# Kernel optimization log

Measured on AMD Instinct MI355X. Metric: run time of the kernel, lower is better.

Reference implementation:

```python
import jax, jax.numpy as jnp
import numpy as np

COST_CLASS, COST_BBOX, COST_GIOU = 2.0, 5.0, 2.0
ALPHA, GAMMA, EPS = 0.25, 2.0, 1e-8


def box_cxcywh_to_xyxy(b):
    cx, cy, w, h = b[..., 0], b[..., 1], b[..., 2], b[..., 3]
    return jnp.stack([cx - 0.5 * w, cy - 0.5 * h, cx + 0.5 * w, cy + 0.5 * h], axis=-1)


def generalized_box_iou(boxes1, boxes2):
    # boxes1: [N,4] xyxy, boxes2: [M,4] xyxy -> [N,M]
    area1 = (boxes1[:, 2] - boxes1[:, 0]) * (boxes1[:, 3] - boxes1[:, 1])
    area2 = (boxes2[:, 2] - boxes2[:, 0]) * (boxes2[:, 3] - boxes2[:, 1])
    lt = jnp.maximum(boxes1[:, None, :2], boxes2[None, :, :2])
    rb = jnp.minimum(boxes1[:, None, 2:], boxes2[None, :, 2:])
    wh = jnp.clip(rb - lt, 0.0)
    inter = wh[..., 0] * wh[..., 1]
    union = area1[:, None] + area2[None, :] - inter
    iou = inter / union
    lt_c = jnp.minimum(boxes1[:, None, :2], boxes2[None, :, :2])
    rb_c = jnp.maximum(boxes1[:, None, 2:], boxes2[None, :, 2:])
    wh_c = jnp.clip(rb_c - lt_c, 0.0)
    area_c = wh_c[..., 0] * wh_c[..., 1]
    return iou - (area_c - union) / area_c


def setup_inputs() -> dict:
    key = jax.random.key(0)
    k1, k2, k3, k4 = jax.random.split(key, 4)
    return {
        "pred_logits": jax.random.normal(k1, (16, 1000, 256), dtype=jnp.float32),
        "pred_boxes": jax.random.uniform(k2, (16, 1000, 4), dtype=jnp.float32),
        "tgt_labels": jax.random.randint(k3, (1600,), 0, 256, dtype=jnp.int64),
        "tgt_boxes": jax.random.uniform(k4, (1600, 4), dtype=jnp.float32),
    }


def reference(pred_logits, pred_boxes, tgt_labels, tgt_boxes):
    """Computes the [bs, num_queries, M] Hungarian cost matrix C.

    The sequential CPU scipy linear_sum_assignment on C is the post-processing
    step; the kernel-relevant math is the fused cost-matrix construction below.
    """
    bs, nq, nc = pred_logits.shape
    out_prob = jax.nn.sigmoid(pred_logits.reshape(bs * nq, nc))  # [N, C]
    out_bbox = pred_boxes.reshape(bs * nq, 4)                    # [N, 4]
    tgt_ids = jnp.clip(tgt_labels, 0, nc - 1)

    # sigmoid focal class cost
    neg_cost = (1.0 - ALPHA) * out_prob**GAMMA * -jnp.log(1.0 - out_prob + EPS)
    pos_cost = ALPHA * (1.0 - out_prob)**GAMMA * -jnp.log(out_prob + EPS)
    cost_class = pos_cost[:, tgt_ids] - neg_cost[:, tgt_ids]     # [N, M]

    # L1 cdist on cxcywh boxes
    cost_bbox = jnp.abs(out_bbox[:, None, :] - tgt_boxes[None, :, :]).sum(-1)

    # negative generalized IoU
    cost_giou = -generalized_box_iou(box_cxcywh_to_xyxy(out_bbox),
                                     box_cxcywh_to_xyxy(tgt_boxes))

    C = COST_BBOX * cost_bbox + COST_CLASS * cost_class + COST_GIOU * cost_giou
    return C.reshape(bs, nq, -1)
```

## Files before the change

kernel.cpp:

```cpp
#include <hip/hip_runtime.h>


constexpr float ALPHAc = 0.25f;
constexpr float EPSc   = 1e-8f;

constexpr int NC  = 256;
constexpr int NT  = 256;
constexpr int RPB = 8;

typedef float f32x4 __attribute__((ext_vector_type(4)));
typedef float f32x2 __attribute__((ext_vector_type(2)));

struct TBox { float x0, y0, x1, y1, area; };

__device__ __forceinline__ TBox make_box(float4 b) {
    TBox r;
    r.x0 = fmaf(-0.5f, b.z, b.x);
    r.y0 = fmaf(-0.5f, b.w, b.y);
    r.x1 = fmaf( 0.5f, b.z, b.x);
    r.y1 = fmaf( 0.5f, b.w, b.y);
    r.area = b.z * b.w;
    return r;
}

__device__ __forceinline__ const float* fc_base(const float* fc0, int c) {
    c = c < 0 ? 0 : (c > NC - 1 ? NC - 1 : c);
    return fc0 + c;
}

__device__ __forceinline__ float cost_elem(float px0, float py0, float px1, float py1,
                                           float parea, float pw2, float ph2,
                                           const TBox& b, float fcp) {
    const float u0 = b.x0 - px0, u1 = b.x1 - px1;
    const float v0 = b.y0 - py0, v1 = b.y1 - py1;
    const float du = u1 - u0,    dv = v1 - v0;
    const float l1 = fmaf(0.5f, fabsf(u0 + u1), fabsf(du))
                   + fmaf(0.5f, fabsf(v0 + v1), fabsf(dv));
    const float ix0 = fmaxf(px0, b.x0), ix1 = fminf(px1, b.x1);
    const float iy0 = fmaxf(py0, b.y0), iy1 = fminf(py1, b.y1);
    const float iwr = ix1 - ix0, ihr = iy1 - iy0;
    const float inter = fmaxf(iwr, 0.0f) * fmaxf(ihr, 0.0f);
    const float uni   = (parea + b.area) - inter;
    const float cw = (pw2 + du) - iwr;
    const float ch = (ph2 + dv) - ihr;
    const float carea = cw * ch;
    const float num = fmaf(uni, uni, inter * carea);
    const float mm  = num * __builtin_amdgcn_rcpf(uni * carea);
    return fmaf(-2.0f, mm, fmaf(5.0f, l1, fcp));
}

__global__ __launch_bounds__(NT)
void hungarian_cost_kernel(const float* __restrict__ logits,
                           const float* __restrict__ pboxes,
                           const int*   __restrict__ tlabels,
                           const float* __restrict__ tboxes,
                           float*       __restrict__ out,
                           int N, int M)
{
    const int t  = threadIdx.x;
    const int n0 = blockIdx.x * RPB;
    if (n0 >= N) return;
    const int rows = (N - n0 < RPB) ? (N - n0) : RPB;

    __shared__ float fc[RPB][NC];
    __shared__ float pp[RPB][8];

#pragma unroll
    for (int r = 0; r < RPB; ++r) {
        if (r < rows) {
            const float x = logits[(size_t)(n0 + r) * NC + t];
            const float p = __builtin_amdgcn_rcpf(1.0f + __expf(-x));
            const float q = 1.0f - p;
            const float pos = ALPHAc * q * q * (-__logf(p + EPSc));
            const float neg = (1.0f - ALPHAc) * p * p * (-__logf(q + EPSc));
            fc[r][t] = fmaf(2.0f, pos - neg, 2.0f);
        }
    }
    if (t < rows) {
        const float4 pb = reinterpret_cast<const float4*>(pboxes)[n0 + t];
        pp[t][0] = fmaf(-0.5f, pb.z, pb.x);
        pp[t][1] = fmaf(-0.5f, pb.w, pb.y);
        pp[t][2] = fmaf( 0.5f, pb.z, pb.x);
        pp[t][3] = fmaf( 0.5f, pb.w, pb.y);
        pp[t][4] = pb.z * pb.w;
        pp[t][5] = pb.z + pb.z;
        pp[t][6] = pb.w + pb.w;
        pp[t][7] = 0.0f;
    }
    __syncthreads();

    const float4* tb4 = reinterpret_cast<const float4*>(tboxes);
    const float*  fc0 = &fc[0][0];

    const int nA    = (M >> 2) < NT ? (M >> 2) : NT;
    const int baseB = 4 * nA;
    const int nB    = ((M - baseB) >> 1) < NT ? ((M - baseB) >> 1) : NT;
    const int baseC = baseB + 2 * nB;

    if (rows == RPB) {

        if (t < nA) {
            const int4 c4 = reinterpret_cast<const int4*>(tlabels)[t];
            const TBox b0 = make_box(tb4[4 * t + 0]);
            const TBox b1 = make_box(tb4[4 * t + 1]);
            const TBox b2 = make_box(tb4[4 * t + 2]);
            const TBox b3 = make_box(tb4[4 * t + 3]);
            const float* g0 = fc_base(fc0, c4.x);
            const float* g1 = fc_base(fc0, c4.y);
            const float* g2 = fc_base(fc0, c4.z);
            const float* g3 = fc_base(fc0, c4.w);
            float fA[RPB][4];
#pragma unroll
            for (int r = 0; r < RPB; ++r) {
                fA[r][0] = g0[r * NC];
                fA[r][1] = g1[r * NC];
                fA[r][2] = g2[r * NC];
                fA[r][3] = g3[r * NC];
            }
#pragma unroll
            for (int r = 0; r < RPB; ++r) {
                const float4 p0 = *reinterpret_cast<const float4*>(&pp[r][0]);
                const float4 p1 = *reinterpret_cast<const float4*>(&pp[r][4]);
                f32x4 res;
                res.x = cost_elem(p0.x, p0.y, p0.z, p0.w, p1.x, p1.y, p1.z, b0, fA[r][0]);
                res.y = cost_elem(p0.x, p0.y, p0.z, p0.w, p1.x, p1.y, p1.z, b1, fA[r][1]);
                res.z = cost_elem(p0.x, p0.y, p0.z, p0.w, p1.x, p1.y, p1.z, b2, fA[r][2]);
                res.w = cost_elem(p0.x, p0.y, p0.z, p0.w, p1.x, p1.y, p1.z, b3, fA[r][3]);
                float* orow = out + (size_t)(n0 + r) * M;
                __builtin_nontemporal_store(res, reinterpret_cast<f32x4*>(orow) + t);
            }
        }

        if (t < nB) {
            const int2 c2 = reinterpret_cast<const int2*>(tlabels + baseB)[t];
            const TBox b0 = make_box(tb4[baseB + 2 * t + 0]);
            const TBox b1 = make_box(tb4[baseB + 2 * t + 1]);
            const float* g0 = fc_base(fc0, c2.x);
            const float* g1 = fc_base(fc0, c2.y);
            float fB[RPB][2];
#pragma unroll
            for (int r = 0; r < RPB; ++r) {
                fB[r][0] = g0[r * NC];
                fB[r][1] = g1[r * NC];
            }
#pragma unroll
            for (int r = 0; r < RPB; ++r) {
                const float4 p0 = *reinterpret_cast<const float4*>(&pp[r][0]);
                const float4 p1 = *reinterpret_cast<const float4*>(&pp[r][4]);
                f32x2 res;
                res.x = cost_elem(p0.x, p0.y, p0.z, p0.w, p1.x, p1.y, p1.z, b0, fB[r][0]);
                res.y = cost_elem(p0.x, p0.y, p0.z, p0.w, p1.x, p1.y, p1.z, b1, fB[r][1]);
                float* orow = out + (size_t)(n0 + r) * M + baseB;
                __builtin_nontemporal_store(res, reinterpret_cast<f32x2*>(orow) + t);
            }
        }

        if (baseC + t < M) {
            const int e = baseC + t;
            const TBox b = make_box(tb4[e]);
            const float* g = fc_base(fc0, tlabels[e]);
            float fC[RPB];
#pragma unroll
            for (int r = 0; r < RPB; ++r) fC[r] = g[r * NC];
#pragma unroll
            for (int r = 0; r < RPB; ++r) {
                const float4 p0 = *reinterpret_cast<const float4*>(&pp[r][0]);
                const float4 p1 = *reinterpret_cast<const float4*>(&pp[r][4]);
                const float v = cost_elem(p0.x, p0.y, p0.z, p0.w, p1.x, p1.y, p1.z, b, fC[r]);
                __builtin_nontemporal_store(v, out + (size_t)(n0 + r) * M + e);
            }
        }
        for (int e = baseC + NT + t; e < M; e += NT) {
            const TBox b = make_box(tb4[e]);
            const float* g = fc_base(fc0, tlabels[e]);
#pragma unroll
            for (int r = 0; r < RPB; ++r) {
                const float4 p0 = *reinterpret_cast<const float4*>(&pp[r][0]);
                const float4 p1 = *reinterpret_cast<const float4*>(&pp[r][4]);
                const float v = cost_elem(p0.x, p0.y, p0.z, p0.w, p1.x, p1.y, p1.z, b, g[r * NC]);
                __builtin_nontemporal_store(v, out + (size_t)(n0 + r) * M + e);
            }
        }
    } else {
        for (int r = 0; r < rows; ++r) {
            const float4 p0 = *reinterpret_cast<const float4*>(&pp[r][0]);
            const float4 p1 = *reinterpret_cast<const float4*>(&pp[r][4]);
            for (int e = t; e < M; e += NT) {
                const TBox b = make_box(tb4[e]);
                const float f = *fc_base(fc0 + r * NC, tlabels[e]);
                out[(size_t)(n0 + r) * M + e] =
                    cost_elem(p0.x, p0.y, p0.z, p0.w, p1.x, p1.y, p1.z, b, f);
            }
        }
    }
}

extern "C" void kernel_launch(void* const* d_in, const int* in_sizes, int n_in,
                              void* d_out, int out_size, void* d_ws, size_t ws_size,
                              hipStream_t stream) {
    const float* logits  = (const float*)d_in[0];
    const float* pboxes  = (const float*)d_in[1];
    const int*   tlabels = (const int*)d_in[2];
    const float* tboxes  = (const float*)d_in[3];

    float* out = (float*)d_out;

    const int N = in_sizes[1] / 4;
    const int M = in_sizes[2];

    const int nblocks = (N + RPB - 1) / RPB;
    hipLaunchKernelGGL(hungarian_cost_kernel, dim3(nblocks), dim3(NT), 0, stream,
                       logits, pboxes, tlabels, tboxes, out, N, M);
}
```

Baseline: 33.26 us.

## Make cost kernel persistent with double-buffered tiles and prefetched logits

Turns the one-block-per-8-rows launch into a persistent grid capped at 500 workgroups. Each block loops over row tiles, keeps target boxes and labels in registers across tiles, and prefetches the next tile's logits and pred boxes into registers while computing the current one. The class-cost shared buffer is double-buffered so a single barrier per tile is enough. This is meant to remove repeated per-block setup and hide global-load latency, at the cost of more registers (possibly lower occupancy) and fewer blocks (N=16000 gives 2000 tiles, so about 4 tiles per block).

```diff
diff --git a/kernel.cpp b/kernel.cpp
--- a/kernel.cpp
+++ b/kernel.cpp
@@ -4,9 +4,10 @@
 constexpr float ALPHAc = 0.25f;
 constexpr float EPSc   = 1e-8f;
 
-constexpr int NC  = 256;
-constexpr int NT  = 256;
-constexpr int RPB = 8;
+constexpr int NC    = 256;
+constexpr int NT    = 256;
+constexpr int RPB   = 8;
+constexpr int MAXWG = 500;
 
 typedef float f32x4 __attribute__((ext_vector_type(4)));
 typedef float f32x2 __attribute__((ext_vector_type(2)));
@@ -23,9 +24,8 @@
     return r;
 }
 
-__device__ __forceinline__ const float* fc_base(const float* fc0, int c) {
-    c = c < 0 ? 0 : (c > NC - 1 ? NC - 1 : c);
-    return fc0 + c;
+__device__ __forceinline__ int clamp_cls(int c) {
+    return c < 0 ? 0 : (c > NC - 1 ? NC - 1 : c);
 }
 
 __device__ __forceinline__ float cost_elem(float px0, float py0, float px1, float py1,
@@ -57,141 +57,207 @@
                            float*       __restrict__ out,
                            int N, int M)
 {
-    const int t  = threadIdx.x;
-    const int n0 = blockIdx.x * RPB;
-    if (n0 >= N) return;
-    const int rows = (N - n0 < RPB) ? (N - n0) : RPB;
-
-    __shared__ float fc[RPB][NC];
-    __shared__ float pp[RPB][8];
-
-#pragma unroll
-    for (int r = 0; r < RPB; ++r) {
-        if (r < rows) {
-            const float x = logits[(size_t)(n0 + r) * NC + t];
-            const float p = __builtin_amdgcn_rcpf(1.0f + __expf(-x));
-            const float q = 1.0f - p;
-            const float pos = ALPHAc * q * q * (-__logf(p + EPSc));
-            const float neg = (1.0f - ALPHAc) * p * p * (-__logf(q + EPSc));
-            fc[r][t] = fmaf(2.0f, pos - neg, 2.0f);
-        }
-    }
-    if (t < rows) {
-        const float4 pb = reinterpret_cast<const float4*>(pboxes)[n0 + t];
-        pp[t][0] = fmaf(-0.5f, pb.z, pb.x);
-        pp[t][1] = fmaf(-0.5f, pb.w, pb.y);
-        pp[t][2] = fmaf( 0.5f, pb.z, pb.x);
-        pp[t][3] = fmaf( 0.5f, pb.w, pb.y);
-        pp[t][4] = pb.z * pb.w;
-        pp[t][5] = pb.z + pb.z;
-        pp[t][6] = pb.w + pb.w;
-        pp[t][7] = 0.0f;
-    }
-    __syncthreads();
+    const int t        = threadIdx.x;
+    const int nwg      = gridDim.x;
+    const int numTiles = (N + RPB - 1) / RPB;
+
+    __shared__ float fc[2][RPB][NC];
+    __shared__ float pp[2][RPB][8];
 
     const float4* tb4 = reinterpret_cast<const float4*>(tboxes);
-    const float*  fc0 = &fc[0][0];
+    const float4* pb4 = reinterpret_cast<const float4*>(pboxes);
 
     const int nA    = (M >> 2) < NT ? (M >> 2) : NT;
     const int baseB = 4 * nA;
     const int nB    = ((M - baseB) >> 1) < NT ? ((M - baseB) >> 1) : NT;
     const int baseC = baseB + 2 * nB;
-
-    if (rows == RPB) {
-
-        if (t < nA) {
-            const int4 c4 = reinterpret_cast<const int4*>(tlabels)[t];
-            const TBox b0 = make_box(tb4[4 * t + 0]);
-            const TBox b1 = make_box(tb4[4 * t + 1]);
-            const TBox b2 = make_box(tb4[4 * t + 2]);
-            const TBox b3 = make_box(tb4[4 * t + 3]);
-            const float* g0 = fc_base(fc0, c4.x);
-            const float* g1 = fc_base(fc0, c4.y);
-            const float* g2 = fc_base(fc0, c4.z);
-            const float* g3 = fc_base(fc0, c4.w);
-            float fA[RPB][4];
+    const bool aV = t < nA;
+    const bool bV = t < nB;
+    const bool cV = (baseC + t) < M;
+
+    TBox bA0 = {}, bA1 = {}, bA2 = {}, bA3 = {}, bB0 = {}, bB1 = {}, bC = {};
+    int cA0 = 0, cA1 = 0, cA2 = 0, cA3 = 0, cB0 = 0, cB1 = 0, cC = 0;
+    if (aV) {
+        const int4 c4 = reinterpret_cast<const int4*>(tlabels)[t];
+        bA0 = make_box(tb4[4 * t + 0]);
+        bA1 = make_box(tb4[4 * t + 1]);
+        bA2 = make_box(tb4[4 * t + 2]);
+        bA3 = make_box(tb4[4 * t + 3]);
+        cA0 = clamp_cls(c4.x); cA1 = clamp_cls(c4.y);
+        cA2 = clamp_cls(c4.z); cA3 = clamp_cls(c4.w);
+    }
+    if (bV) {
+        const int2 c2 = reinterpret_cast<const int2*>(tlabels + baseB)[t];
+        bB0 = make_box(tb4[baseB + 2 * t + 0]);
+        bB1 = make_box(tb4[baseB + 2 * t + 1]);
+        cB0 = clamp_cls(c2.x); cB1 = clamp_cls(c2.y);
+    }
+    if (cV) {
+        bC = make_box(tb4[baseC + t]);
+        cC = clamp_cls(tlabels[baseC + t]);
+    }
+
+    int tile = blockIdx.x;
+    if (tile >= numTiles) return;
+
+    float xcur[RPB];
+    float4 pbcur = {0.0f, 0.0f, 0.0f, 0.0f};
+    {
+        const int n0 = tile * RPB;
+#pragma unroll
+        for (int r = 0; r < RPB; ++r) {
+            int n = n0 + r; n = n < N - 1 ? n : N - 1;
+            xcur[r] = logits[(size_t)n * NC + t];
+        }
+        if (t < RPB) {
+            int n = n0 + t; n = n < N - 1 ? n : N - 1;
+            pbcur = pb4[n];
+        }
+    }
+
+    bool bsel = false;
+    for (; tile < numTiles; tile += nwg) {
+        const int n0   = tile * RPB;
+        const int rows = (N - n0 < RPB) ? (N - n0) : RPB;
+        float (*fcb)[NC] = bsel ? fc[1] : fc[0];
+        float (*ppb)[8]  = bsel ? pp[1] : pp[0];
+
+#pragma unroll
+        for (int r = 0; r < RPB; ++r) {
+            if (r < rows) {
+                const float x = xcur[r];
+                const float p = __builtin_amdgcn_rcpf(1.0f + __expf(-x));
+                const float q = 1.0f - p;
+                const float pos = ALPHAc * q * q * (-__logf(p + EPSc));
+                const float neg = (1.0f - ALPHAc) * p * p * (-__logf(q + EPSc));
+                fcb[r][t] = fmaf(2.0f, pos - neg, 2.0f);
+            }
+        }
+        if (t < rows) {
+            const float4 pb = pbcur;
+            ppb[t][0] = fmaf(-0.5f, pb.z, pb.x);
+            ppb[t][1] = fmaf(-0.5f, pb.w, pb.y);
+            ppb[t][2] = fmaf( 0.5f, pb.z, pb.x);
+            ppb[t][3] = fmaf( 0.5f, pb.w, pb.y);
+            ppb[t][4] = pb.z * pb.w;
+            ppb[t][5] = pb.z + pb.z;
+            ppb[t][6] = pb.w + pb.w;
+            ppb[t][7] = 0.0f;
+        }
+        __syncthreads();
+
+        const int ntile = tile + nwg;
+        float xnext[RPB];
+        float4 pbnext = pbcur;
+        if (ntile < numTiles) {
+            const int nn0 = ntile * RPB;
 #pragma unroll
             for (int r = 0; r < RPB; ++r) {
-                fA[r][0] = g0[r * NC];
-                fA[r][1] = g1[r * NC];
-                fA[r][2] = g2[r * NC];
-                fA[r][3] = g3[r * NC];
-            }
-#pragma unroll
-            for (int r = 0; r < RPB; ++r) {
-                const float4 p0 = *reinterpret_cast<const float4*>(&pp[r][0]);
-                const float4 p1 = *reinterpret_cast<const float4*>(&pp[r][4]);
-                f32x4 res;
-                res.x = cost_elem(p0.x, p0.y, p0.z, p0.w, p1.x, p1.y, p1.z, b0, fA[r][0]);
-                res.y = cost_elem(p0.x, p0.y, p0.z, p0.w, p1.x, p1.y, p1.z, b1, fA[r][1]);
-                res.z = cost_elem(p0.x, p0.y, p0.z, p0.w, p1.x, p1.y, p1.z, b2, fA[r][2]);
-                res.w = cost_elem(p0.x, p0.y, p0.z, p0.w, p1.x, p1.y, p1.z, b3, fA[r][3]);
-                float* orow = out + (size_t)(n0 + r) * M;
-                __builtin_nontemporal_store(res, reinterpret_cast<f32x4*>(orow) + t);
-            }
-        }
-
-        if (t < nB) {
-            const int2 c2 = reinterpret_cast<const int2*>(tlabels + baseB)[t];
-            const TBox b0 = make_box(tb4[baseB + 2 * t + 0]);
-            const TBox b1 = make_box(tb4[baseB + 2 * t + 1]);
-            const float* g0 = fc_base(fc0, c2.x);
-            const float* g1 = fc_base(fc0, c2.y);
-            float fB[RPB][2];
-#pragma unroll
-            for (int r = 0; r < RPB; ++r) {
-                fB[r][0] = g0[r * NC];
-                fB[r][1] = g1[r * NC];
-            }
-#pragma unroll
-            for (int r = 0; r < RPB; ++r) {
-                const float4 p0 = *reinterpret_cast<const float4*>(&pp[r][0]);
-                const float4 p1 = *reinterpret_cast<const float4*>(&pp[r][4]);
-                f32x2 res;
-                res.x = cost_elem(p0.x, p0.y, p0.z, p0.w, p1.x, p1.y, p1.z, b0, fB[r][0]);
-                res.y = cost_elem(p0.x, p0.y, p0.z, p0.w, p1.x, p1.y, p1.z, b1, fB[r][1]);
-                float* orow = out + (size_t)(n0 + r) * M + baseB;
-                __builtin_nontemporal_store(res, reinterpret_cast<f32x2*>(orow) + t);
-            }
-        }
-
-        if (baseC + t < M) {
-            const int e = baseC + t;
-            const TBox b = make_box(tb4[e]);
-            const float* g = fc_base(fc0, tlabels[e]);
-            float fC[RPB];
-#pragma unroll
-            for (int r = 0; r < RPB; ++r) fC[r] = g[r * NC];
-#pragma unroll
-            for (int r = 0; r < RPB; ++r) {
-                const float4 p0 = *reinterpret_cast<const float4*>(&pp[r][0]);
-                const float4 p1 = *reinterpret_cast<const float4*>(&pp[r][4]);
-                const float v = cost_elem(p0.x, p0.y, p0.z, p0.w, p1.x, p1.y, p1.z, b, fC[r]);
-                __builtin_nontemporal_store(v, out + (size_t)(n0 + r) * M + e);
-            }
-        }
-        for (int e = baseC + NT + t; e < M; e += NT) {
-            const TBox b = make_box(tb4[e]);
-            const float* g = fc_base(fc0, tlabels[e]);
-#pragma unroll
-            for (int r = 0; r < RPB; ++r) {
-                const float4 p0 = *reinterpret_cast<const float4*>(&pp[r][0]);
-                const float4 p1 = *reinterpret_cast<const float4*>(&pp[r][4]);
-                const float v = cost_elem(p0.x, p0.y, p0.z, p0.w, p1.x, p1.y, p1.z, b, g[r * NC]);
-                __builtin_nontemporal_store(v, out + (size_t)(n0 + r) * M + e);
-            }
-        }
-    } else {
-        for (int r = 0; r < rows; ++r) {
-            const float4 p0 = *reinterpret_cast<const float4*>(&pp[r][0]);
-            const float4 p1 = *reinterpret_cast<const float4*>(&pp[r][4]);
-            for (int e = t; e < M; e += NT) {
+                int n = nn0 + r; n = n < N - 1 ? n : N - 1;
+                xnext[r] = logits[(size_t)n * NC + t];
+            }
+            if (t < RPB) {
+                int n = nn0 + t; n = n < N - 1 ? n : N - 1;
+                pbnext = pb4[n];
+            }
+        } else {
+#pragma unroll
+            for (int r = 0; r < RPB; ++r) xnext[r] = 0.0f;
+        }
+
+        const float* fr = &fcb[0][0];
+
+        if (rows == RPB) {
+            if (aV) {
+                const float* g0 = fr + cA0;
+                const float* g1 = fr + cA1;
+                const float* g2 = fr + cA2;
+                const float* g3 = fr + cA3;
+                float fA[RPB][4];
+#pragma unroll
+                for (int r = 0; r < RPB; ++r) {
+                    fA[r][0] = g0[r * NC];
+                    fA[r][1] = g1[r * NC];
+                    fA[r][2] = g2[r * NC];
+                    fA[r][3] = g3[r * NC];
+                }
+#pragma unroll
+                for (int r = 0; r < RPB; ++r) {
+                    const float4 p0 = *reinterpret_cast<const float4*>(&ppb[r][0]);
+                    const float4 p1 = *reinterpret_cast<const float4*>(&ppb[r][4]);
+                    f32x4 res;
+                    res.x = cost_elem(p0.x, p0.y, p0.z, p0.w, p1.x, p1.y, p1.z, bA0, fA[r][0]);
+                    res.y = cost_elem(p0.x, p0.y, p0.z, p0.w, p1.x, p1.y, p1.z, bA1, fA[r][1]);
+                    res.z = cost_elem(p0.x, p0.y, p0.z, p0.w, p1.x, p1.y, p1.z, bA2, fA[r][2]);
+                    res.w = cost_elem(p0.x, p0.y, p0.z, p0.w, p1.x, p1.y, p1.z, bA3, fA[r][3]);
+                    float* orow = out + (size_t)(n0 + r) * M;
+                    __builtin_nontemporal_store(res, reinterpret_cast<f32x4*>(orow) + t);
+                }
+            }
+
+            if (bV) {
+                const float* g0 = fr + cB0;
+                const float* g1 = fr + cB1;
+                float fB[RPB][2];
+#pragma unroll
+                for (int r = 0; r < RPB; ++r) {
+                    fB[r][0] = g0[r * NC];
+                    fB[r][1] = g1[r * NC];
+                }
+#pragma unroll
+                for (int r = 0; r < RPB; ++r) {
+                    const float4 p0 = *reinterpret_cast<const float4*>(&ppb[r][0]);
+                    const float4 p1 = *reinterpret_cast<const float4*>(&ppb[r][4]);
+                    f32x2 res;
+                    res.x = cost_elem(p0.x, p0.y, p0.z, p0.w, p1.x, p1.y, p1.z, bB0, fB[r][0]);
+                    res.y = cost_elem(p0.x, p0.y, p0.z, p0.w, p1.x, p1.y, p1.z, bB1, fB[r][1]);
+                    float* orow = out + (size_t)(n0 + r) * M + baseB;
+                    __builtin_nontemporal_store(res, reinterpret_cast<f32x2*>(orow) + t);
+                }
+            }
+
+            if (cV) {
+                const int e = baseC + t;
+                const float* g = fr + cC;
+                float fCv[RPB];
+#pragma unroll
+                for (int r = 0; r < RPB; ++r) fCv[r] = g[r * NC];
+#pragma unroll
+                for (int r = 0; r < RPB; ++r) {
+                    const float4 p0 = *reinterpret_cast<const float4*>(&ppb[r][0]);
+                    const float4 p1 = *reinterpret_cast<const float4*>(&ppb[r][4]);
+                    const float v = cost_elem(p0.x, p0.y, p0.z, p0.w, p1.x, p1.y, p1.z, bC, fCv[r]);
+                    __builtin_nontemporal_store(v, out + (size_t)(n0 + r) * M + e);
+                }
+            }
+            for (int e = baseC + NT + t; e < M; e += NT) {
                 const TBox b = make_box(tb4[e]);
-                const float f = *fc_base(fc0 + r * NC, tlabels[e]);
-                out[(size_t)(n0 + r) * M + e] =
-                    cost_elem(p0.x, p0.y, p0.z, p0.w, p1.x, p1.y, p1.z, b, f);
-            }
-        }
+                const float* g = fr + clamp_cls(tlabels[e]);
+#pragma unroll
+                for (int r = 0; r < RPB; ++r) {
+                    const float4 p0 = *reinterpret_cast<const float4*>(&ppb[r][0]);
+                    const float4 p1 = *reinterpret_cast<const float4*>(&ppb[r][4]);
+                    const float v = cost_elem(p0.x, p0.y, p0.z, p0.w, p1.x, p1.y, p1.z, b, g[r * NC]);
+                    __builtin_nontemporal_store(v, out + (size_t)(n0 + r) * M + e);
+                }
+            }
+        } else {
+            for (int r = 0; r < rows; ++r) {
+                const float4 p0 = *reinterpret_cast<const float4*>(&ppb[r][0]);
+                const float4 p1 = *reinterpret_cast<const float4*>(&ppb[r][4]);
+                for (int e = t; e < M; e += NT) {
+                    const TBox b = make_box(tb4[e]);
+                    const float f = fr[clamp_cls(tlabels[e]) + r * NC];
+                    out[(size_t)(n0 + r) * M + e] =
+                        cost_elem(p0.x, p0.y, p0.z, p0.w, p1.x, p1.y, p1.z, b, f);
+                }
+            }
+        }
+
+#pragma unroll
+        for (int r = 0; r < RPB; ++r) xcur[r] = xnext[r];
+        pbcur = pbnext;
+        bsel = !bsel;
     }
 }
 
@@ -208,7 +274,8 @@
     const int N = in_sizes[1] / 4;
     const int M = in_sizes[2];
 
-    const int nblocks = (N + RPB - 1) / RPB;
+    const int numTiles = (N + RPB - 1) / RPB;
+    const int nblocks  = numTiles < MAXWG ? numTiles : MAXWG;
     hipLaunchKernelGGL(hungarian_cost_kernel, dim3(nblocks), dim3(NT), 0, stream,
                        logits, pboxes, tlabels, tboxes, out, N, M);
 }
```

Result: slower. 42.95 us (+29.1%).
